# Kernel optimization log

Hardware: AMD Instinct MI355X
Metric: run time of the kernel (lower is better)

Reference implementation:

```python
import jax, jax.numpy as jnp
import numpy as np

IRR_IN = 4
IRR_OUT = 4
N_SCALAR = 64
E = 1_000_000
DIM = IRR_IN * IRR_OUT * 2  # 32
HID = 2 * DIM               # 64

# ir_1: swap-pair gather index [1,0,3,2,5,4,7,6]
IR_1 = np.concatenate([np.array([1, 0]) + 2 * i for i in range(IRR_IN)])
# ir_2: alternating sign [1,-1,1,-1,...]
IR_2 = np.ones(2 * IRR_IN, dtype=np.float32)
IR_2[1::2] = -1.0


def setup_inputs() -> dict:
    key = jax.random.key(0)
    ks = jax.random.split(key, 4)
    x = jax.random.normal(ks[0], (E, IRR_IN, 2), dtype=jnp.float32)
    s = jax.random.normal(ks[1], (E, N_SCALAR), dtype=jnp.float32)
    W1 = jax.random.normal(ks[2], (N_SCALAR, HID), dtype=jnp.float32) * (1.0 / np.sqrt(N_SCALAR))
    b1 = jnp.zeros((HID,), dtype=jnp.float32)
    W2 = jax.random.normal(ks[3], (HID, DIM), dtype=jnp.float32) * (1.0 / np.sqrt(HID))
    b2 = jnp.zeros((DIM,), dtype=jnp.float32)
    return {"x": x, "s": s, "W1": W1, "b1": b1, "W2": W2, "b2": b2}


def reference(x, s, W1, b1, W2, b2):
    ir1 = jnp.asarray(IR_1)
    ir2 = jnp.asarray(IR_2)
    # per-edge MLP producing raw weights: [E, irr_out, 2*irr_in]
    h = jax.nn.relu(s @ W1 + b1)
    w = (h @ W2 + b2).reshape(-1, IRR_OUT, 2 * IRR_IN)
    w_1 = w[:, :, ir1]        # pair-swapped copy
    w_2 = w * ir2             # sign-alternated copy
    # stack -> [E, 2, irr_out, 2*irr_in]; permute -> [E, 2*irr_in, irr_out, 2]
    wm = jnp.stack((w_2, w_1), axis=1).transpose(0, 3, 2, 1)
    wm = wm.reshape(-1, 2 * IRR_IN, 2 * IRR_OUT)  # [E, 2*irr_in, 2*irr_out]
    xf = x.reshape(-1, 2 * IRR_IN)                # [E, 2*irr_in]
    out = jnp.einsum('ei,eio->eo', xf, wm)        # tiny per-edge matvec
    return out.reshape(-1, IRR_OUT, 2)
```

## Files before the change

kernel.cpp:

```cpp
#include <hip/hip_runtime.h>
#include <hip/hip_bf16.h>

typedef __bf16 bf16x8 __attribute__((ext_vector_type(8)));
typedef __bf16 bf16x4 __attribute__((ext_vector_type(4)));
typedef float  f32x4  __attribute__((ext_vector_type(4)));
typedef float  f32x2  __attribute__((ext_vector_type(2)));

#define MFMA16(A, B, C) __builtin_amdgcn_mfma_f32_16x16x32_bf16(A, B, C, 0, 0, 0)
#define FENCE_WAIT() do { asm volatile("s_waitcnt lgkmcnt(0)" ::: "memory"); \
                          __builtin_amdgcn_sched_barrier(0); } while (0)
#define FENCE_COMPILER() asm volatile("" ::: "memory")

__global__ __launch_bounds__(256, 4) void so2_fused_kernel(
    const float* __restrict__ x, const float* __restrict__ s,
    const float* __restrict__ W1, const float* __restrict__ b1v,
    const float* __restrict__ W2, const float* __restrict__ b2v,
    float* __restrict__ out, int E)
{
  __shared__ unsigned short lds_w1t[64 * 64];
  __shared__ unsigned short lds_w2t[32 * 64];
  __shared__ char lds_h[4][2048];

  const int tid  = threadIdx.x;
  const int wid  = tid >> 6;
  const int lane = tid & 63;
  const int lrow = lane & 15;
  const int lg   = lane >> 4;

  f32x4 bias1[4], bias2[2];
  #pragma unroll
  for (int jt = 0; jt < 4; ++jt) bias1[jt] = *(const f32x4*)(b1v + jt * 16 + lg * 4);
  #pragma unroll
  for (int dt = 0; dt < 2; ++dt) bias2[dt] = *(const f32x4*)(b2v + dt * 16 + lg * 4);

  #pragma unroll
  for (int it = 0; it < 4; ++it) {
    int i = (it * 256 + tid) * 4;
    f32x4 v = *(const f32x4*)(W1 + i);
    int k = i >> 6, j = i & 63;
    #pragma unroll
    for (int q = 0; q < 4; ++q) {
      int byte = ((j + q) << 7) + (k << 1);
      byte ^= ((j + q) & 7) << 4;
      *(unsigned short*)((char*)lds_w1t + byte) =
          __builtin_bit_cast(unsigned short, (__bf16)v[q]);
    }
  }
  #pragma unroll
  for (int it = 0; it < 2; ++it) {
    int i = (it * 256 + tid) * 4;
    f32x4 v = *(const f32x4*)(W2 + i);
    int k = i >> 5, d = i & 31;
    #pragma unroll
    for (int q = 0; q < 4; ++q) {
      int byte = ((d + q) << 7) + (k << 1);
      byte ^= ((d + q) & 7) << 4;
      *(unsigned short*)((char*)lds_w2t + byte) =
          __builtin_bit_cast(unsigned short, (__bf16)v[q]);
    }
  }
  __syncthreads();

  bf16x8 w2f[2][2];
  #pragma unroll
  for (int dt = 0; dt < 2; ++dt)
    #pragma unroll
    for (int c = 0; c < 2; ++c) {
      int d = dt * 16 + lrow;
      int byte = (d << 7) + ((c * 32 + lg * 8) << 1);
      byte ^= (d & 7) << 4;
      w2f[dt][c] = *(const bf16x8*)((const char*)lds_w2t + byte);
    }

  const int wbase = blockIdx.x * 512 + wid * 128;
  const int rem = E - wbase;
  const int nt = rem <= 0 ? 0 : (rem >= 128 ? 8 : ((rem + 15) >> 4));
  if (nt == 0) return;

  char* hbuf = lds_h[wid];

  f32x4 sN[4];
  f32x4 xN;
  {
    int er = wbase + lrow; er = er < E ? er : E - 1;
    const float* sp = s + (size_t)er * 64 + lg * 8;
    sN[0] = *(const f32x4*)(sp);
    sN[1] = *(const f32x4*)(sp + 4);
    sN[2] = *(const f32x4*)(sp + 32);
    sN[3] = *(const f32x4*)(sp + 36);
    xN = *(const f32x4*)(x + (size_t)er * 8 + (lg & 1) * 4);
  }

  for (int t = 0; t < nt; ++t) {
    const int ebase = wbase + t * 16;

    bf16x8 sf0, sf1;
    #pragma unroll
    for (int i = 0; i < 4; ++i) {
      sf0[i] = (__bf16)sN[0][i]; sf0[i + 4] = (__bf16)sN[1][i];
      sf1[i] = (__bf16)sN[2][i]; sf1[i + 4] = (__bf16)sN[3][i];
    }
    const f32x4 xe = xN;

    {
      int er = ebase + 16 + lrow; er = er < E ? er : E - 1;
      const float* sp = s + (size_t)er * 64 + lg * 8;
      sN[0] = *(const f32x4*)(sp);
      sN[1] = *(const f32x4*)(sp + 4);
      sN[2] = *(const f32x4*)(sp + 32);
      sN[3] = *(const f32x4*)(sp + 36);
      xN = *(const f32x4*)(x + (size_t)er * 8 + (lg & 1) * 4);
    }

    #pragma unroll
    for (int jt = 0; jt < 4; ++jt) {
      const int j = jt * 16 + lrow;
      int wb0 = (j << 7) + ((lg * 8) << 1);      wb0 ^= (j & 7) << 4;
      int wb1 = (j << 7) + ((32 + lg * 8) << 1); wb1 ^= (j & 7) << 4;
      bf16x8 wf0 = *(const bf16x8*)((const char*)lds_w1t + wb0);
      bf16x8 wf1 = *(const bf16x8*)((const char*)lds_w1t + wb1);
      f32x4 acc = bias1[jt];
      acc = MFMA16(wf0, sf0, acc);
      acc = MFMA16(wf1, sf1, acc);
      bf16x4 hv;
      #pragma unroll
      for (int r = 0; r < 4; ++r) hv[r] = (__bf16)fmaxf(acc[r], 0.f);
      int byte = (lrow << 7) + ((jt * 16 + lg * 4) << 1);
      byte ^= (lrow & 7) << 4;
      *(bf16x4*)(hbuf + byte) = hv;
    }

    FENCE_WAIT();

    bf16x8 hf0, hf1;
    {
      int b0 = (lrow << 7) + ((lg * 8) << 1);      b0 ^= (lrow & 7) << 4;
      int b1 = (lrow << 7) + ((32 + lg * 8) << 1); b1 ^= (lrow & 7) << 4;
      hf0 = *(const bf16x8*)(hbuf + b0);
      hf1 = *(const bf16x8*)(hbuf + b1);
    }
    FENCE_COMPILER();

    float qr[2], qi[2];
    #pragma unroll
    for (int dt = 0; dt < 2; ++dt) {
      f32x4 a = bias2[dt];
      a = MFMA16(w2f[dt][0], hf0, a);
      a = MFMA16(w2f[dt][1], hf1, a);
      float pr = xe[0] * a[0] - xe[1] * a[1] + xe[2] * a[2] - xe[3] * a[3];
      float pi = xe[0] * a[1] + xe[1] * a[0] + xe[2] * a[3] + xe[3] * a[2];
      qr[dt] = pr + __shfl_xor(pr, 16, 64);
      qi[dt] = pi + __shfl_xor(pi, 16, 64);
    }
    const int sel = lg & 1;
    const int o = (lg >> 1) + 2 * sel;
    const float vr = sel ? qr[1] : qr[0];
    const float vi = sel ? qi[1] : qi[0];
    const int e = ebase + lrow;
    if (e < E) {
      f32x2 v2 = {vr, vi};
      *(f32x2*)(out + (size_t)e * 8 + o * 2) = v2;
    }
  }
}

extern "C" void kernel_launch(void* const* d_in, const int* in_sizes, int n_in,
                              void* d_out, int out_size, void* d_ws, size_t ws_size,
                              hipStream_t stream) {
  const float* x  = (const float*)d_in[0];
  const float* s  = (const float*)d_in[1];
  const float* W1 = (const float*)d_in[2];
  const float* b1 = (const float*)d_in[3];
  const float* W2 = (const float*)d_in[4];
  const float* b2 = (const float*)d_in[5];
  float* out = (float*)d_out;
  const int E = in_sizes[0] / 8;
  const int blocks = (E + 511) / 512;
  so2_fused_kernel<<<blocks, 256, 0, stream>>>(x, s, W1, b1, W2, b2, out, E);
}
```

Before: 61.45 us.

## Feed layer-1 MFMA output directly into K16 MFMAs, skipping LDS round-trip

When a 16x16x16 bf16 MFMA builtin is available, the hidden activations from the first MFMA layer stay in registers and feed the second layer as four K=16 MFMAs. This works because the first layer's output layout already matches the K16 operand layout, so the per-tile LDS write, wait and read-back of h goes away. The code also hoists the first s/x prefetch ahead of the weight staging so global loads overlap the LDS setup. The trade-off is twice as many second-layer MFMA instructions at half the K depth, and the fast path depends on compile-time builtin detection.

New measurement: 60.88 us. Within noise of the previous version (-0.9%).

```diff
diff --git a/kernel.cpp b/kernel.cpp
--- a/kernel.cpp
+++ b/kernel.cpp
@@ -6,7 +6,18 @@
 typedef float  f32x4  __attribute__((ext_vector_type(4)));
 typedef float  f32x2  __attribute__((ext_vector_type(2)));
 
-#define MFMA16(A, B, C) __builtin_amdgcn_mfma_f32_16x16x32_bf16(A, B, C, 0, 0, 0)
+#define MFMA32(A, B, C) __builtin_amdgcn_mfma_f32_16x16x32_bf16(A, B, C, 0, 0, 0)
+
+#if __has_builtin(__builtin_amdgcn_mfma_f32_16x16x16bf16_1k)
+  #define HAVE_MFMA_K16 1
+  #define MFMA16(A, B, C) __builtin_amdgcn_mfma_f32_16x16x16bf16_1k(A, B, C, 0, 0, 0)
+#elif __has_builtin(__builtin_amdgcn_mfma_f32_16x16x16_bf16)
+  #define HAVE_MFMA_K16 1
+  #define MFMA16(A, B, C) __builtin_amdgcn_mfma_f32_16x16x16_bf16(A, B, C, 0, 0, 0)
+#else
+  #define HAVE_MFMA_K16 0
+#endif
+
 #define FENCE_WAIT() do { asm volatile("s_waitcnt lgkmcnt(0)" ::: "memory"); \
                           __builtin_amdgcn_sched_barrier(0); } while (0)
 #define FENCE_COMPILER() asm volatile("" ::: "memory")
@@ -19,7 +30,9 @@
 {
   __shared__ unsigned short lds_w1t[64 * 64];
   __shared__ unsigned short lds_w2t[32 * 64];
+#if !HAVE_MFMA_K16
   __shared__ char lds_h[4][2048];
+#endif
 
   const int tid  = threadIdx.x;
   const int wid  = tid >> 6;
@@ -27,62 +40,13 @@
   const int lrow = lane & 15;
   const int lg   = lane >> 4;
 
-  f32x4 bias1[4], bias2[2];
-  #pragma unroll
-  for (int jt = 0; jt < 4; ++jt) bias1[jt] = *(const f32x4*)(b1v + jt * 16 + lg * 4);
-  #pragma unroll
-  for (int dt = 0; dt < 2; ++dt) bias2[dt] = *(const f32x4*)(b2v + dt * 16 + lg * 4);
-
-  #pragma unroll
-  for (int it = 0; it < 4; ++it) {
-    int i = (it * 256 + tid) * 4;
-    f32x4 v = *(const f32x4*)(W1 + i);
-    int k = i >> 6, j = i & 63;
-    #pragma unroll
-    for (int q = 0; q < 4; ++q) {
-      int byte = ((j + q) << 7) + (k << 1);
-      byte ^= ((j + q) & 7) << 4;
-      *(unsigned short*)((char*)lds_w1t + byte) =
-          __builtin_bit_cast(unsigned short, (__bf16)v[q]);
-    }
-  }
-  #pragma unroll
-  for (int it = 0; it < 2; ++it) {
-    int i = (it * 256 + tid) * 4;
-    f32x4 v = *(const f32x4*)(W2 + i);
-    int k = i >> 5, d = i & 31;
-    #pragma unroll
-    for (int q = 0; q < 4; ++q) {
-      int byte = ((d + q) << 7) + (k << 1);
-      byte ^= ((d + q) & 7) << 4;
-      *(unsigned short*)((char*)lds_w2t + byte) =
-          __builtin_bit_cast(unsigned short, (__bf16)v[q]);
-    }
-  }
-  __syncthreads();
-
-  bf16x8 w2f[2][2];
-  #pragma unroll
-  for (int dt = 0; dt < 2; ++dt)
-    #pragma unroll
-    for (int c = 0; c < 2; ++c) {
-      int d = dt * 16 + lrow;
-      int byte = (d << 7) + ((c * 32 + lg * 8) << 1);
-      byte ^= (d & 7) << 4;
-      w2f[dt][c] = *(const bf16x8*)((const char*)lds_w2t + byte);
-    }
-
   const int wbase = blockIdx.x * 512 + wid * 128;
-  const int rem = E - wbase;
-  const int nt = rem <= 0 ? 0 : (rem >= 128 ? 8 : ((rem + 15) >> 4));
-  if (nt == 0) return;
-
-  char* hbuf = lds_h[wid];
 
   f32x4 sN[4];
   f32x4 xN;
   {
-    int er = wbase + lrow; er = er < E ? er : E - 1;
+    int er = wbase + lrow; er = (unsigned)er < (unsigned)E ? er : E - 1;
+    if (er < 0) er = 0;
     const float* sp = s + (size_t)er * 64 + lg * 8;
     sN[0] = *(const f32x4*)(sp);
     sN[1] = *(const f32x4*)(sp + 4);
@@ -90,6 +54,72 @@
     sN[3] = *(const f32x4*)(sp + 36);
     xN = *(const f32x4*)(x + (size_t)er * 8 + (lg & 1) * 4);
   }
+
+  f32x4 bias1[4], bias2[2];
+  #pragma unroll
+  for (int jt = 0; jt < 4; ++jt) bias1[jt] = *(const f32x4*)(b1v + jt * 16 + lg * 4);
+  #pragma unroll
+  for (int dt = 0; dt < 2; ++dt) bias2[dt] = *(const f32x4*)(b2v + dt * 16 + lg * 4);
+
+  #pragma unroll
+  for (int it = 0; it < 4; ++it) {
+    int i = (it * 256 + tid) * 4;
+    f32x4 v = *(const f32x4*)(W1 + i);
+    int k = i >> 6, j = i & 63;
+    #pragma unroll
+    for (int q = 0; q < 4; ++q) {
+      int byte = ((j + q) << 7) + (k << 1);
+      byte ^= ((j + q) & 7) << 4;
+      *(unsigned short*)((char*)lds_w1t + byte) =
+          __builtin_bit_cast(unsigned short, (__bf16)v[q]);
+    }
+  }
+  #pragma unroll
+  for (int it = 0; it < 2; ++it) {
+    int i = (it * 256 + tid) * 4;
+    f32x4 v = *(const f32x4*)(W2 + i);
+    int k = i >> 5, d = i & 31;
+    #pragma unroll
+    for (int q = 0; q < 4; ++q) {
+      int byte = ((d + q) << 7) + (k << 1);
+      byte ^= ((d + q) & 7) << 4;
+      *(unsigned short*)((char*)lds_w2t + byte) =
+          __builtin_bit_cast(unsigned short, (__bf16)v[q]);
+    }
+  }
+  __syncthreads();
+
+#if HAVE_MFMA_K16
+  bf16x4 w2q[2][4];
+  #pragma unroll
+  for (int dt = 0; dt < 2; ++dt)
+    #pragma unroll
+    for (int kt = 0; kt < 4; ++kt) {
+      int d = dt * 16 + lrow;
+      int byte = (d << 7) + ((kt * 16 + lg * 4) << 1);
+      byte ^= (d & 7) << 4;
+      w2q[dt][kt] = *(const bf16x4*)((const char*)lds_w2t + byte);
+    }
+#else
+  bf16x8 w2f[2][2];
+  #pragma unroll
+  for (int dt = 0; dt < 2; ++dt)
+    #pragma unroll
+    for (int c = 0; c < 2; ++c) {
+      int d = dt * 16 + lrow;
+      int byte = (d << 7) + ((c * 32 + lg * 8) << 1);
+      byte ^= (d & 7) << 4;
+      w2f[dt][c] = *(const bf16x8*)((const char*)lds_w2t + byte);
+    }
+#endif
+
+  const int rem = E - wbase;
+  const int nt = rem <= 0 ? 0 : (rem >= 128 ? 8 : ((rem + 15) >> 4));
+  if (nt == 0) return;
+
+#if !HAVE_MFMA_K16
+  char* hbuf = lds_h[wid];
+#endif
 
   for (int t = 0; t < nt; ++t) {
     const int ebase = wbase + t * 16;
@@ -112,6 +142,8 @@
       xN = *(const f32x4*)(x + (size_t)er * 8 + (lg & 1) * 4);
     }
 
+#if HAVE_MFMA_K16
+    bf16x4 hq[4];
     #pragma unroll
     for (int jt = 0; jt < 4; ++jt) {
       const int j = jt * 16 + lrow;
@@ -120,8 +152,34 @@
       bf16x8 wf0 = *(const bf16x8*)((const char*)lds_w1t + wb0);
       bf16x8 wf1 = *(const bf16x8*)((const char*)lds_w1t + wb1);
       f32x4 acc = bias1[jt];
-      acc = MFMA16(wf0, sf0, acc);
-      acc = MFMA16(wf1, sf1, acc);
+      acc = MFMA32(wf0, sf0, acc);
+      acc = MFMA32(wf1, sf1, acc);
+      #pragma unroll
+      for (int r = 0; r < 4; ++r) hq[jt][r] = (__bf16)fmaxf(acc[r], 0.f);
+    }
+
+    float qr[2], qi[2];
+    #pragma unroll
+    for (int dt = 0; dt < 2; ++dt) {
+      f32x4 a = bias2[dt];
+      #pragma unroll
+      for (int kt = 0; kt < 4; ++kt) a = MFMA16(w2q[dt][kt], hq[kt], a);
+      float pr = xe[0] * a[0] - xe[1] * a[1] + xe[2] * a[2] - xe[3] * a[3];
+      float pi = xe[0] * a[1] + xe[1] * a[0] + xe[2] * a[3] + xe[3] * a[2];
+      qr[dt] = pr + __shfl_xor(pr, 16, 64);
+      qi[dt] = pi + __shfl_xor(pi, 16, 64);
+    }
+#else
+    #pragma unroll
+    for (int jt = 0; jt < 4; ++jt) {
+      const int j = jt * 16 + lrow;
+      int wb0 = (j << 7) + ((lg * 8) << 1);      wb0 ^= (j & 7) << 4;
+      int wb1 = (j << 7) + ((32 + lg * 8) << 1); wb1 ^= (j & 7) << 4;
+      bf16x8 wf0 = *(const bf16x8*)((const char*)lds_w1t + wb0);
+      bf16x8 wf1 = *(const bf16x8*)((const char*)lds_w1t + wb1);
+      f32x4 acc = bias1[jt];
+      acc = MFMA32(wf0, sf0, acc);
+      acc = MFMA32(wf1, sf1, acc);
       bf16x4 hv;
       #pragma unroll
       for (int r = 0; r < 4; ++r) hv[r] = (__bf16)fmaxf(acc[r], 0.f);
@@ -129,9 +187,7 @@
       byte ^= (lrow & 7) << 4;
       *(bf16x4*)(hbuf + byte) = hv;
     }
-
     FENCE_WAIT();
-
     bf16x8 hf0, hf1;
     {
       int b0 = (lrow << 7) + ((lg * 8) << 1);      b0 ^= (lrow & 7) << 4;
@@ -140,18 +196,19 @@
       hf1 = *(const bf16x8*)(hbuf + b1);
     }
     FENCE_COMPILER();
-
     float qr[2], qi[2];
     #pragma unroll
     for (int dt = 0; dt < 2; ++dt) {
       f32x4 a = bias2[dt];
-      a = MFMA16(w2f[dt][0], hf0, a);
-      a = MFMA16(w2f[dt][1], hf1, a);
+      a = MFMA32(w2f[dt][0], hf0, a);
+      a = MFMA32(w2f[dt][1], hf1, a);
       float pr = xe[0] * a[0] - xe[1] * a[1] + xe[2] * a[2] - xe[3] * a[3];
       float pi = xe[0] * a[1] + xe[1] * a[0] + xe[2] * a[3] + xe[3] * a[2];
       qr[dt] = pr + __shfl_xor(pr, 16, 64);
       qi[dt] = pi + __shfl_xor(pi, 16, 64);
     }
+#endif
+
     const int sel = lg & 1;
     const int o = (lg >> 1) + 2 * sel;
     const float vr = sel ? qr[1] : qr[0];
```
